# Kernel tuning notes

Hardware: AMD Instinct MI355X
Metric: run time of the kernel (lower is better)

Reference implementation:

```python
import jax, jax.numpy as jnp
import numpy as np

L, D, H, DFF = 4, 1024, 16, 4096
DH = D // H
B, T = 2, 2048
EPS = 1e-5


def setup_inputs() -> dict:
    key = jax.random.key(0)
    ks = jax.random.split(key, 16)
    xav_a = (6.0 / (D + D)) ** 0.5      # xavier_uniform for square DxD
    xav_f1 = (6.0 / (D + DFF)) ** 0.5
    xav_f2 = (6.0 / (DFF + D)) ** 0.5
    def u(k, shape, a):
        return jax.random.uniform(k, shape, jnp.float32, -a, a)
    inp = {
        "x": jax.random.normal(ks[0], (B, T, D), jnp.float32),
        "mask": jnp.ones((B, T), jnp.int32),
        # attention projections, torch Linear layout [out, in]
        "Wq": u(ks[1], (L, D, D), xav_a), "bq": jnp.zeros((L, D), jnp.float32),
        "Wk": u(ks[2], (L, D, D), xav_a), "bk": jnp.zeros((L, D), jnp.float32),
        "Wv": u(ks[3], (L, D, D), xav_a), "bv": jnp.zeros((L, D), jnp.float32),
        "Wo": u(ks[4], (L, D, D), xav_a), "bo": jnp.zeros((L, D), jnp.float32),
        # FFN
        "fc1_w": u(ks[5], (L, DFF, D), xav_f1), "fc1_b": jnp.zeros((L, DFF), jnp.float32),
        "fc2_w": u(ks[6], (L, D, DFF), xav_f2), "fc2_b": jnp.zeros((L, D), jnp.float32),
        # LayerNorms
        "ln1_g": jnp.ones((L, D), jnp.float32), "ln1_b": jnp.zeros((L, D), jnp.float32),
        "ln2_g": jnp.ones((L, D), jnp.float32), "ln2_b": jnp.zeros((L, D), jnp.float32),
        "lnf_g": jnp.ones((D,), jnp.float32), "lnf_b": jnp.zeros((D,), jnp.float32),
    }
    return inp


def _layernorm(x, g, b):
    mu = jnp.mean(x, axis=-1, keepdims=True)
    var = jnp.mean(jnp.square(x - mu), axis=-1, keepdims=True)
    return (x - mu) * jax.lax.rsqrt(var + EPS) * g + b


def _encoder_forward(x, mask, Wq, bq, Wk, bk, Wv, bv, Wo, bo,
                     fc1_w, fc1_b, fc2_w, fc2_b,
                     ln1_g, ln1_b, ln2_g, ln2_b, lnf_g, lnf_b):
    keep = mask.astype(bool)[:, None, None, :]  # [B,1,1,Tk]
    scale = 1.0 / (DH ** 0.5)
    for l in range(L):
        # --- multi-head self-attention ---
        q = (jnp.einsum('btd,ed->bte', x, Wq[l]) + bq[l]).reshape(B, T, H, DH).transpose(0, 2, 1, 3)
        k = (jnp.einsum('btd,ed->bte', x, Wk[l]) + bk[l]).reshape(B, T, H, DH).transpose(0, 2, 1, 3)
        v = (jnp.einsum('btd,ed->bte', x, Wv[l]) + bv[l]).reshape(B, T, H, DH).transpose(0, 2, 1, 3)
        logits = jnp.einsum('bhqd,bhkd->bhqk', q, k) * scale
        logits = jnp.where(keep, logits, -jnp.inf)
        attn = jax.nn.softmax(logits, axis=-1)
        ctx = jnp.einsum('bhqk,bhkd->bhqd', attn, v).transpose(0, 2, 1, 3).reshape(B, T, D)
        attn_out = jnp.einsum('btd,ed->bte', ctx, Wo[l]) + bo[l]
        x = _layernorm(x + attn_out, ln1_g[l], ln1_b[l])
        # --- feed-forward (exact GELU, like torch nn.GELU default) ---
        h = jax.nn.gelu(jnp.einsum('btd,fd->btf', x, fc1_w[l]) + fc1_b[l], approximate=False)
        ff_out = jnp.einsum('btf,df->btd', h, fc2_w[l]) + fc2_b[l]
        x = _layernorm(x + ff_out, ln2_g[l], ln2_b[l])
    return _layernorm(x, lnf_g, lnf_b)


def reference(x, mask, Wq, bq, Wk, bk, Wv, bv, Wo, bo,
              fc1_w, fc1_b, fc2_w, fc2_b,
              ln1_g, ln1_b, ln2_g, ln2_b, lnf_g, lnf_b):
    return _encoder_forward(x, mask, Wq, bq, Wk, bk, Wv, bv, Wo, bo,
                            fc1_w, fc1_b, fc2_w, fc2_b,
                            ln1_g, ln1_b, ln2_g, ln2_b, lnf_g, lnf_b)
```

## Files before the change

kernel.cpp:

```cpp
#include <hip/hip_runtime.h>
#include <hip/hip_bf16.h>
#include <cstdint>

#define BB 2
#define TT 2048
#define DD 1024
#define HH 16
#define DHH 64
#define DFF 4096
#define LL 4
#define MM (BB*TT)
#define NT (TT/64)

typedef __attribute__((ext_vector_type(8))) short short8v;
typedef __attribute__((ext_vector_type(4))) short short4v;
typedef __attribute__((ext_vector_type(4))) float floatx4;

typedef __attribute__((address_space(3))) void lds_void;
typedef const __attribute__((address_space(1))) void glb_void;

__device__ __forceinline__ void gload_lds16(const void* g, void* l) {
  __builtin_amdgcn_global_load_lds((glb_void*)g, (lds_void*)l, 16, 0, 0);
}

__device__ __forceinline__ float bf2f(short s) {
  union { unsigned u; float f; } v; v.u = ((unsigned)(unsigned short)s) << 16; return v.f;
}
__device__ __forceinline__ short f2bf(float f) {
  union { float f; unsigned u; } v; v.f = f;
  unsigned r = (v.u + 0x7fffu + ((v.u >> 16) & 1u)) >> 16;
  return (short)r;
}
__device__ __forceinline__ unsigned pack2bf(float a, float b) {
  __hip_bfloat162 h = __float22bfloat162_rn(make_float2(a, b));
  return *reinterpret_cast<unsigned*>(&h);
}
__device__ __forceinline__ float fexp2(float x) {
  float r; asm("v_exp_f32 %0, %1" : "=v"(r) : "v"(x)); return r;
}
__device__ __forceinline__ float max3f(float a, float b, float c) {
  float r; asm("v_max3_f32 %0, %1, %2, %3" : "=v"(r) : "v"(a), "v"(b), "v"(c)); return r;
}
__device__ __forceinline__ float gelu_fast(float x) {
  const float u = x * x;
  const float w = fmaf(u, -0.10294537f, -2.302203f);
  const float t = fexp2(w * x);
  return x * __builtin_amdgcn_rcpf(1.f + t);
}

#define SCL2 0.18033688011112042f
__device__ __forceinline__ short8v scale8(short8v v) {
  short8v r;
#pragma unroll
  for (int i = 0; i < 8; ++i) r[i] = f2bf(bf2f(v[i]) * SCL2);
  return r;
}

#define SEG (DD*DD)
#define WTOT (4*SEG + 2*DFF*DD)
__global__ __launch_bounds__(256) void cast_layer(
    const float* __restrict__ wq, const float* __restrict__ wk,
    const float* __restrict__ wv, const float* __restrict__ wo,
    const float* __restrict__ f1, const float* __restrict__ f2,
    short* __restrict__ dst)
{
  const int i = (blockIdx.x * 256 + threadIdx.x) * 4;
  const float* src; int off;
  if      (i <     SEG) { src = wq; off = i; }
  else if (i < 2 * SEG) { src = wk; off = i - SEG; }
  else if (i < 3 * SEG) { src = wv; off = i - 2 * SEG; }
  else if (i < 4 * SEG) { src = wo; off = i - 3 * SEG; }
  else if (i < 4 * SEG + DFF * DD) { src = f1; off = i - 4 * SEG; }
  else { src = f2; off = i - 4 * SEG - DFF * DD; }
  const float4 v = *(const float4*)(src + off);
  short4v o; o[0] = f2bf(v.x); o[1] = f2bf(v.y); o[2] = f2bf(v.z); o[3] = f2bf(v.w);
  *(short4v*)(dst + i) = o;
}

template<int GELU, int QKV>
__global__ __launch_bounds__(512, 2) void gemm256(
    const short* __restrict__ A, const short* __restrict__ W,
    const float* __restrict__ b0, const float* __restrict__ b1,
    const float* __restrict__ b2, short* __restrict__ C,
    int M, int N, int K)
{
  __shared__ __align__(16) short lds[65536];
  const int t = threadIdx.x;
  const int lane = t & 63, wave = t >> 6;
  const int wm = wave >> 2, wn = wave & 3;
  const int l15 = lane & 15, lg = lane >> 4;

  const int nwg = gridDim.x * gridDim.y;
  const int bid0 = blockIdx.y * gridDim.x + blockIdx.x;
  const int q8 = nwg >> 3;
  const int lid = (bid0 & 7) * q8 + (bid0 >> 3);
  const int bx = lid % gridDim.x, by = lid / gridDim.x;

  const size_t abase = (size_t)by * 256 * K;
  const size_t wbase = (size_t)bx * 256 * K;

  floatx4 acc[8][4];
  floatx4 zero = {0.f, 0.f, 0.f, 0.f};
#pragma unroll
  for (int m = 0; m < 8; ++m)
#pragma unroll
    for (int n = 0; n < 4; ++n) acc[m][n] = zero;

#define STG_A(sl_, h_, u_) do {                                                \
    _Pragma("unroll")                                                          \
    for (int j_ = 0; j_ < 2; ++j_) {                                           \
      const int c_ = j_ * 512 + t, r_ = c_ >> 3;                               \
      const int kc_ = (c_ & 7) ^ (r_ & 7);                                     \
      gload_lds16(A + abase + (size_t)((h_) * 128 + r_) * K + (u_) * 64 + kc_ * 8, \
                  &lds[(sl_) * 16384 + (h_) * 8192 + (j_ * 512 + wave * 64) * 8]); \
    } } while (0)
#define STG_B(sl_, h_, u_) do {                                                \
    _Pragma("unroll")                                                          \
    for (int j_ = 0; j_ < 2; ++j_) {                                           \
      const int c_ = j_ * 512 + t, r_ = c_ >> 3;                               \
      const int kc_ = (c_ & 7) ^ (r_ & 7);                                     \
      gload_lds16(W + wbase + (size_t)((h_) * 128 + r_) * K + (u_) * 64 + kc_ * 8, \
                  &lds[32768 + (sl_) * 16384 + (h_) * 8192 + (j_ * 512 + wave * 64) * 8]); \
    } } while (0)

  const int NTK = K >> 6;
  STG_A(0, 0, 0); STG_A(0, 1, 0); STG_B(0, 0, 0); STG_B(0, 1, 0);

  for (int u = 0; u < NTK; ++u) {
    const int sl = u & 1, ns = sl ^ 1;
    const int aoff = sl * 16384 + wm * 8192;
    const int boff = 32768 + sl * 16384 + (wn >> 1) * 8192;
    short8v bfr[4][2];
#pragma unroll
    for (int p = 0; p < 4; ++p) {
      if (p == 0) {
        if (u + 1 < NTK) {
          STG_A(ns, 0, u + 1);
          asm volatile("s_waitcnt vmcnt(2)" ::: "memory");
        } else {
          asm volatile("s_waitcnt vmcnt(0)" ::: "memory");
        }
        __builtin_amdgcn_s_barrier();
#pragma unroll
        for (int n = 0; n < 4; ++n)
#pragma unroll
          for (int kk = 0; kk < 2; ++kk) {
            const int rl = (wn & 1) * 64 + n * 16 + l15;
            bfr[n][kk] = *(const short8v*)&lds[boff + rl * 64 + ((kk * 4 + lg) ^ (rl & 7)) * 8];
          }
      } else if (p == 1) { if (u + 1 < NTK) STG_A(ns, 1, u + 1); }
      else if (p == 2)   { if (u + 1 < NTK) STG_B(ns, 0, u + 1); }
      else               { if (u + 1 < NTK) STG_B(ns, 1, u + 1); }

      short8v af[2][2];
#pragma unroll
      for (int i = 0; i < 2; ++i)
#pragma unroll
        for (int kk = 0; kk < 2; ++kk) {
          const int rl = (2 * p + i) * 16 + l15;
          af[i][kk] = *(const short8v*)&lds[aoff + rl * 64 + ((kk * 4 + lg) ^ (rl & 7)) * 8];
        }
      asm volatile("s_waitcnt lgkmcnt(0)" ::: "memory");
      __builtin_amdgcn_s_setprio(1);
#pragma unroll
      for (int kk = 0; kk < 2; ++kk)
#pragma unroll
        for (int i = 0; i < 2; ++i)
#pragma unroll
          for (int n = 0; n < 4; ++n)
            acc[2 * p + i][n] = __builtin_amdgcn_mfma_f32_16x16x32_bf16(
                af[i][kk], bfr[n][kk], acc[2 * p + i][n], 0, 0, 0);
      __builtin_amdgcn_s_setprio(0);
      __builtin_amdgcn_s_barrier();
    }
  }
#undef STG_A
#undef STG_B

  const float* bp;
  int cbase = bx * 256 + wn * 64;
  if (QKV) {
    const int seg = cbase >> 10;
    bp = (seg == 0) ? b0 : (seg == 1 ? b1 : b2);
    cbase -= seg << 10;
  } else {
    bp = b0;
  }
  float bv[4];
#pragma unroll
  for (int n = 0; n < 4; ++n)
    bv[n] = bp[cbase + n * 16 + l15];
#pragma unroll
  for (int m = 0; m < 8; ++m)
#pragma unroll
    for (int jj = 0; jj < 4; ++jj) {
      const int row = by * 256 + wm * 128 + m * 16 + lg * 4 + jj;
      short* cp = C + (size_t)row * N + bx * 256 + wn * 64 + l15;
#pragma unroll
      for (int n = 0; n < 4; ++n) {
        float v = acc[m][n][jj] + bv[n];
        if (GELU) v = gelu_fast(v);
        cp[n * 16] = f2bf(v);
      }
    }
}

template<int GELU>
__global__ __launch_bounds__(512, 2) void gemm128(
    const short* __restrict__ A, const short* __restrict__ W,
    const float* __restrict__ bias, short* __restrict__ C,
    int M, int N, int K)
{
  __shared__ __align__(16) short lds[49152];
  const int t = threadIdx.x;
  const int lane = t & 63, wave = t >> 6;
  const int wm = wave >> 2, wn = wave & 3;
  const int l15 = lane & 15, lg = lane >> 4;

  const int nwg = gridDim.x * gridDim.y;
  const int bid0 = blockIdx.y * gridDim.x + blockIdx.x;
  const int q8 = nwg >> 3;
  const int lid = (bid0 & 7) * q8 + (bid0 >> 3);
  const int bx = lid % gridDim.x, by = lid / gridDim.x;

  const size_t abase = (size_t)by * 128 * K;
  const size_t wbase = (size_t)bx * 128 * K;

  floatx4 acc[4][2];
  floatx4 zero = {0.f, 0.f, 0.f, 0.f};
#pragma unroll
  for (int m = 0; m < 4; ++m)
#pragma unroll
    for (int n = 0; n < 2; ++n) acc[m][n] = zero;

#define STG128(sl_, u_) do {                                                   \
    _Pragma("unroll")                                                          \
    for (int j_ = 0; j_ < 2; ++j_) {                                           \
      const int c_ = j_ * 512 + t, r_ = c_ >> 3;                               \
      const int kc_ = (c_ & 7) ^ (r_ & 7);                                     \
      gload_lds16(A + abase + (size_t)r_ * K + (u_) * 64 + kc_ * 8,            \
                  &lds[(sl_) * 8192 + (j_ * 512 + wave * 64) * 8]);            \
      gload_lds16(W + wbase + (size_t)r_ * K + (u_) * 64 + kc_ * 8,            \
                  &lds[24576 + (sl_) * 8192 + (j_ * 512 + wave * 64) * 8]);    \
    } } while (0)

  const int NTK = K >> 6;
  STG128(0, 0);
  STG128(1, 1);

  for (int u = 0; u < NTK; ++u) {
    const int sl = u % 3;
    if (u + 1 < NTK) asm volatile("s_waitcnt vmcnt(4)" ::: "memory");
    else             asm volatile("s_waitcnt vmcnt(0)" ::: "memory");
    __builtin_amdgcn_s_barrier();
    if (u + 2 < NTK) STG128((u + 2) % 3, u + 2);

    short8v bfr[2][2], af[4][2];
#pragma unroll
    for (int n = 0; n < 2; ++n)
#pragma unroll
      for (int kk = 0; kk < 2; ++kk) {
        const int rl = wn * 32 + n * 16 + l15;
        bfr[n][kk] = *(const short8v*)&lds[24576 + sl * 8192 + rl * 64 + ((kk * 4 + lg) ^ (rl & 7)) * 8];
      }
#pragma unroll
    for (int m = 0; m < 4; ++m)
#pragma unroll
      for (int kk = 0; kk < 2; ++kk) {
        const int rl = wm * 32 + ((m & 1) * 16) + l15 + (m >> 1) * 64;
        af[m][kk] = *(const short8v*)&lds[sl * 8192 + rl * 64 + ((kk * 4 + lg) ^ (rl & 7)) * 8];
      }
    asm volatile("s_waitcnt lgkmcnt(0)" ::: "memory");
    __builtin_amdgcn_s_setprio(1);
#pragma unroll
    for (int kk = 0; kk < 2; ++kk)
#pragma unroll
      for (int m = 0; m < 4; ++m)
#pragma unroll
        for (int n = 0; n < 2; ++n)
          acc[m][n] = __builtin_amdgcn_mfma_f32_16x16x32_bf16(af[m][kk], bfr[n][kk], acc[m][n], 0, 0, 0);
    __builtin_amdgcn_s_setprio(0);
  }
#undef STG128

  float bv[2];
#pragma unroll
  for (int n = 0; n < 2; ++n)
    bv[n] = bias[bx * 128 + wn * 32 + n * 16 + l15];
#pragma unroll
  for (int m = 0; m < 4; ++m)
#pragma unroll
    for (int jj = 0; jj < 4; ++jj) {
      const int row = by * 128 + wm * 32 + (m & 1) * 16 + (m >> 1) * 64 + lg * 4 + jj;
      short* cp = C + (size_t)row * N + bx * 128 + wn * 32 + l15;
#pragma unroll
      for (int n = 0; n < 2; ++n) {
        float v = acc[m][n][jj] + bv[n];
        if (GELU) v = gelu_fast(v);
        cp[n * 16] = f2bf(v);
      }
    }
}

__global__ __launch_bounds__(256) void transpose_v(
    const short* __restrict__ qkv, short* __restrict__ vt)
{
  __shared__ short tile[64][65];
  const int tb = blockIdx.x, h = blockIdx.y, b = blockIdx.z;
  const int t = threadIdx.x;
  const int r = t >> 2, c4 = (t & 3) * 16;
  const short* src = qkv + ((size_t)(b * TT + tb * 64 + r)) * 3072 + 2048 + h * 64 + c4;
#pragma unroll
  for (int i = 0; i < 16; ++i) tile[r][c4 + i] = src[i];
  __syncthreads();
  short* dst = vt + ((size_t)((b * HH + h) * 64 + r)) * TT + tb * 64 + c4;
#pragma unroll
  for (int i = 0; i < 16; ++i) dst[i] = tile[c4 + i][r];
}

#define PSTR 72
__global__ __launch_bounds__(512, 4) void flash_attn(
    const short* __restrict__ qkv, const short* __restrict__ vt,
    const int* __restrict__ mask, short* __restrict__ ctx)
{
  const int t = threadIdx.x;
  const int lane = t & 63, wave = t >> 6;
  const int l15 = lane & 15, lg = lane >> 4;

  const int bid0 = blockIdx.x + gridDim.x * (blockIdx.y + gridDim.y * blockIdx.z);
  const int lid = (bid0 & 7) * 64 + (bid0 >> 3);
  const int qb = lid & 15, h = (lid >> 4) & 15, b = lid >> 8;

  __shared__ __align__(16) short Ks[2][64 * 64];
  __shared__ __align__(16) short Vs[2][64 * 64];
  __shared__ __align__(16) short p_lds[8][16 * PSTR];
  __shared__ int allv_lds;
  short* prow = p_lds[wave];

  if (t == 0) allv_lds = 1;
  __syncthreads();
  {
    const int4 mv = *(const int4*)&mask[b * TT + t * 4];
    if (!(mv.x && mv.y && mv.z && mv.w)) allv_lds = 0;
  }
  __syncthreads();
  const bool allv = (allv_lds != 0);

  const short* qp = qkv + ((size_t)(b * TT + qb * 128 + wave * 16 + l15)) * 3072 + h * 64;
  const short8v qf0 = scale8(*(const short8v*)(qp + lg * 8));
  const short8v qf1 = scale8(*(const short8v*)(qp + 32 + lg * 8));

  const short* kbase = qkv + (size_t)b * TT * 3072 + 1024 + h * 64;
  const short* vtb   = vt + ((size_t)(b * HH + h)) * 64 * TT;

  const int srow = lane >> 3;
  const int scol = (lane & 7) ^ (srow & 7);

  float m_run = -3e30f, l_run = 0.f;
  floatx4 zero = {0.f, 0.f, 0.f, 0.f};
  floatx4 o[4];
#pragma unroll
  for (int n = 0; n < 4; ++n) o[n] = zero;

#define STAGE_KV(bufi, kb_) do {                                             \
    const int r_ = wave * 8 + srow;                                          \
    gload_lds16(kbase + (size_t)((kb_) * 64 + r_) * 3072 + scol * 8,         \
                &Ks[bufi][wave * 512]);                                      \
    gload_lds16(vtb + (size_t)r_ * TT + (kb_) * 64 + scol * 8,               \
                &Vs[bufi][wave * 512]);                                      \
  } while (0)

#define FLASH_LOOP(MASKED)                                                        \
  {                                                                               \
    STAGE_KV(0, 0);                                                               \
    int buf = 0;                                                                  \
    for (int kb = 0; kb < NT; ++kb) {                                             \
      if (kb + 1 < NT) {                                                          \
        STAGE_KV(buf ^ 1, kb + 1);                                                \
        asm volatile("s_waitcnt vmcnt(2)" ::: "memory");                          \
      } else {                                                                    \
        asm volatile("s_waitcnt vmcnt(0)" ::: "memory");                          \
      }                                                                           \
      __builtin_amdgcn_s_barrier();                                               \
                                                                                  \
      float cm[4][4];                                                             \
      if (MASKED) {                                                               \
        _Pragma("unroll")                                                         \
        for (int n = 0; n < 4; ++n) {                                             \
          const int4 mv = *(const int4*)&mask[b * TT + kb * 64 + n * 16 + lg * 4];\
          cm[n][0] = mv.x ? 0.f : -1.5e30f; cm[n][1] = mv.y ? 0.f : -1.5e30f;     \
          cm[n][2] = mv.z ? 0.f : -1.5e30f; cm[n][3] = mv.w ? 0.f : -1.5e30f;     \
        }                                                                         \
      }                                                                           \
                                                                                  \
      floatx4 s[4];                                                               \
      _Pragma("unroll")                                                           \
      for (int n = 0; n < 4; ++n) {                                               \
        const int row = n * 16 + l15;                                             \
        const int ch0 = lg ^ (row & 7);                                           \
        const int ch1 = (lg + 4) ^ (row & 7);                                     \
        const short8v kf0 = *(const short8v*)&Ks[buf][row * 64 + ch0 * 8];        \
        const short8v kf1 = *(const short8v*)&Ks[buf][row * 64 + ch1 * 8];        \
        floatx4 a = zero;                                                         \
        a = __builtin_amdgcn_mfma_f32_16x16x32_bf16(kf0, qf0, a, 0, 0, 0);        \
        a = __builtin_amdgcn_mfma_f32_16x16x32_bf16(kf1, qf1, a, 0, 0, 0);        \
        s[n] = a;                                                                 \
      }                                                                           \
      if (MASKED) {                                                               \
        _Pragma("unroll")                                                         \
        for (int n = 0; n < 4; ++n)                                               \
          _Pragma("unroll")                                                       \
          for (int jj = 0; jj < 4; ++jj) s[n][jj] += cm[n][jj];                   \
      }                                                                           \
                                                                                  \
      const float t0 = max3f(s[0][0], s[0][1], s[0][2]);                          \
      const float t1 = max3f(s[0][3], s[1][0], s[1][1]);                          \
      const float t2 = max3f(s[1][2], s[1][3], s[2][0]);                          \
      const float t3 = max3f(s[2][1], s[2][2], s[2][3]);                          \
      const float t4 = max3f(s[3][0], s[3][1], s[3][2]);                          \
      float mx = fmaxf(max3f(t0, t1, t2), max3f(t3, t4, s[3][3]));                \
      mx = fmaxf(mx, __shfl_xor(mx, 16, 64));                                     \
      mx = fmaxf(mx, __shfl_xor(mx, 32, 64));                                     \
                                                                                  \
      const bool defer = __all(mx - m_run <= 11.5f);                              \
      const float mnew = defer ? m_run : fmaxf(m_run, mx);                        \
      float ps[4];                                                                \
      _Pragma("unroll")                                                           \
      for (int n = 0; n < 4; ++n) {                                               \
        s[n][0] = fexp2(s[n][0] - mnew);                                          \
        s[n][1] = fexp2(s[n][1] - mnew);                                          \
        s[n][2] = fexp2(s[n][2] - mnew);                                          \
        s[n][3] = fexp2(s[n][3] - mnew);                                          \
        ps[n] = (s[n][0] + s[n][1]) + (s[n][2] + s[n][3]);                        \
      }                                                                           \
      float sum = (ps[0] + ps[1]) + (ps[2] + ps[3]);                              \
      sum += __shfl_xor(sum, 16, 64);                                             \
      sum += __shfl_xor(sum, 32, 64);                                             \
      if (defer) {                                                                \
        l_run += sum;                                                             \
      } else {                                                                    \
        const float al = fexp2(m_run - mnew);                                     \
        l_run = l_run * al + sum;                                                 \
        m_run = mnew;                                                             \
        float alo[4];                                                             \
        _Pragma("unroll")                                                         \
        for (int jj = 0; jj < 4; ++jj) alo[jj] = __shfl(al, lg * 4 + jj, 16);     \
        _Pragma("unroll")                                                         \
        for (int n = 0; n < 4; ++n)                                               \
          _Pragma("unroll")                                                       \
          for (int jj = 0; jj < 4; ++jj) o[n][jj] *= alo[jj];                     \
      }                                                                           \
                                                                                  \
      _Pragma("unroll")                                                           \
      for (int n = 0; n < 4; ++n) {                                               \
        const unsigned u0 = pack2bf(s[n][0], s[n][1]);                            \
        const unsigned u1 = pack2bf(s[n][2], s[n][3]);                            \
        *(uint2*)&prow[l15 * PSTR + n * 16 + lg * 4] = make_uint2(u0, u1);        \
      }                                                                           \
      const short8v pf0 = *(const short8v*)&prow[l15 * PSTR + lg * 8];            \
      const short8v pf1 = *(const short8v*)&prow[l15 * PSTR + 32 + lg * 8];       \
                                                                                  \
      _Pragma("unroll")                                                           \
      for (int n = 0; n < 4; ++n) {                                               \
        const int row = n * 16 + l15;                                             \
        const int ch0 = lg ^ (row & 7);                                           \
        const int ch1 = (lg + 4) ^ (row & 7);                                     \
        const short8v vf0 = *(const short8v*)&Vs[buf][row * 64 + ch0 * 8];        \
        const short8v vf1 = *(const short8v*)&Vs[buf][row * 64 + ch1 * 8];        \
        o[n] = __builtin_amdgcn_mfma_f32_16x16x32_bf16(pf0, vf0, o[n], 0, 0, 0);  \
        o[n] = __builtin_amdgcn_mfma_f32_16x16x32_bf16(pf1, vf1, o[n], 0, 0, 0);  \
      }                                                                           \
      asm volatile("" ::: "memory");                                              \
      __builtin_amdgcn_s_barrier();                                               \
      buf ^= 1;                                                                   \
    }                                                                             \
  }

  if (allv) FLASH_LOOP(0)
  else      FLASH_LOOP(1)
#undef FLASH_LOOP
#undef STAGE_KV

#pragma unroll
  for (int jj = 0; jj < 4; ++jj) {
    const float inv = 1.f / __shfl(l_run, lg * 4 + jj, 16);
    const int row = qb * 128 + wave * 16 + lg * 4 + jj;
#pragma unroll
    for (int n = 0; n < 4; ++n)
      ctx[((size_t)(b * TT + row)) * DD + h * 64 + n * 16 + l15] = f2bf(o[n][jj] * inv);
  }
}

__global__ __launch_bounds__(256) void add_ln(
    const float* __restrict__ xres, const short* __restrict__ add,
    const float* __restrict__ g, const float* __restrict__ bb,
    float* __restrict__ outf, short* __restrict__ outb)
{
  const int row = blockIdx.x, t = threadIdx.x;
  const int lane = t & 63, wave = t >> 6;
  const float4 xv = *(const float4*)(xres + (size_t)row * DD + t * 4);
  float y[4] = { xv.x, xv.y, xv.z, xv.w };
  if (add) {
    const short4v av = *(const short4v*)(add + (size_t)row * DD + t * 4);
#pragma unroll
    for (int i = 0; i < 4; ++i) y[i] += bf2f(av[i]);
  }
  float s = y[0] + y[1] + y[2] + y[3];
  float ss = y[0]*y[0] + y[1]*y[1] + y[2]*y[2] + y[3]*y[3];
#pragma unroll
  for (int off = 32; off >= 1; off >>= 1) {
    s  += __shfl_xor(s, off, 64);
    ss += __shfl_xor(ss, off, 64);
  }
  __shared__ float red[2][4];
  if (lane == 0) { red[0][wave] = s; red[1][wave] = ss; }
  __syncthreads();
  s  = red[0][0] + red[0][1] + red[0][2] + red[0][3];
  ss = red[1][0] + red[1][1] + red[1][2] + red[1][3];
  const float mu = s * (1.f / DD);
  const float var = ss * (1.f / DD) - mu * mu;
  const float rs = rsqrtf(var + 1e-5f);
  const float4 gv = *(const float4*)(g + t * 4);
  const float4 bv = *(const float4*)(bb + t * 4);
  float o[4];
  o[0] = (y[0] - mu) * rs * gv.x + bv.x;
  o[1] = (y[1] - mu) * rs * gv.y + bv.y;
  o[2] = (y[2] - mu) * rs * gv.z + bv.z;
  o[3] = (y[3] - mu) * rs * gv.w + bv.w;
  if (outf) *(float4*)(outf + (size_t)row * DD + t * 4) = make_float4(o[0], o[1], o[2], o[3]);
  if (outb) {
    short4v ov;
#pragma unroll
    for (int i = 0; i < 4; ++i) ov[i] = f2bf(o[i]);
    *(short4v*)(outb + (size_t)row * DD + t * 4) = ov;
  }
}

__global__ __launch_bounds__(256) void cast_in(
    const float* __restrict__ x, short* __restrict__ xb)
{
  const int i = (blockIdx.x * 256 + threadIdx.x) * 4;
  const float4 v = *(const float4*)(x + i);
  short4v o; o[0] = f2bf(v.x); o[1] = f2bf(v.y); o[2] = f2bf(v.z); o[3] = f2bf(v.w);
  *(short4v*)(xb + i) = o;
}

extern "C" void kernel_launch(void* const* d_in, const int* in_sizes, int n_in,
                              void* d_out, int out_size, void* d_ws, size_t ws_size,
                              hipStream_t stream) {
  const float* x   = (const float*)d_in[0];
  const int* mask  = (const int*)d_in[1];
  const float* Wq  = (const float*)d_in[2];
  const float* bq  = (const float*)d_in[3];
  const float* Wk  = (const float*)d_in[4];
  const float* bk  = (const float*)d_in[5];
  const float* Wv  = (const float*)d_in[6];
  const float* bv  = (const float*)d_in[7];
  const float* Wo  = (const float*)d_in[8];
  const float* bo  = (const float*)d_in[9];
  const float* f1w = (const float*)d_in[10];
  const float* f1b = (const float*)d_in[11];
  const float* f2w = (const float*)d_in[12];
  const float* f2b = (const float*)d_in[13];
  const float* l1g = (const float*)d_in[14];
  const float* l1b = (const float*)d_in[15];
  const float* l2g = (const float*)d_in[16];
  const float* l2b = (const float*)d_in[17];
  const float* lfg = (const float*)d_in[18];
  const float* lfb = (const float*)d_in[19];
  float* out = (float*)d_out;

  char* ws = (char*)d_ws;
  const size_t MB = 1u << 20;
  float* xf   = (float*)(ws);
  short* xb   = (short*)(ws + 16 * MB);
  short* qkv  = (short*)(ws + 24 * MB);
  short* vt_  = (short*)(ws + 48 * MB);
  short* ctx  = (short*)(ws + 56 * MB);
  short* tmp  = (short*)(ws + 64 * MB);
  short* wbuf = (short*)(ws + 72 * MB);
  short* hb   = qkv;

  cast_in<<<(MM * DD) / (256 * 4), 256, 0, stream>>>(x, xb);

  for (int l = 0; l < LL; ++l) {
    cast_layer<<<WTOT / (256 * 4), 256, 0, stream>>>(
        Wq + (size_t)l * SEG, Wk + (size_t)l * SEG, Wv + (size_t)l * SEG, Wo + (size_t)l * SEG,
        f1w + (size_t)l * DFF * DD, f2w + (size_t)l * DD * DFF, wbuf);
    const short* wqkv_b = wbuf;
    const short* wo_b   = wbuf + 3 * SEG;
    const short* f1_b   = wbuf + 4 * SEG;
    const short* f2_b   = wbuf + 4 * SEG + DFF * DD;

    gemm256<0,1><<<dim3(3072 / 256, MM / 256), 512, 0, stream>>>(
        xb, wqkv_b, bq + l * DD, bk + l * DD, bv + l * DD, qkv, MM, 3072, DD);
    transpose_v<<<dim3(TT / 64, HH, BB), 256, 0, stream>>>(qkv, vt_);
    flash_attn<<<dim3(TT / 128, HH, BB), 512, 0, stream>>>(qkv, vt_, mask, ctx);
    gemm128<0><<<dim3(DD / 128, MM / 128), 512, 0, stream>>>(ctx, wo_b, bo + l * DD, tmp, MM, DD, DD);
    add_ln<<<MM, 256, 0, stream>>>(l == 0 ? x : xf, tmp, l1g + l * DD, l1b + l * DD, xf, xb);
    gemm256<1,0><<<dim3(DFF / 256, MM / 256), 512, 0, stream>>>(
        xb, f1_b, f1b + l * DFF, nullptr, nullptr, hb, MM, DFF, DD);
    gemm128<0><<<dim3(DD / 128, MM / 128), 512, 0, stream>>>(hb, f2_b, f2b + l * DD, tmp, MM, DD, DFF);
    add_ln<<<MM, 256, 0, stream>>>(xf, tmp, l2g + l * DD, l2b + l * DD, xf, xb);
  }
  add_ln<<<MM, 256, 0, stream>>>(xf, nullptr, lfg, lfb, out, nullptr);
}
```

Before: 907.0 us.

## Fuse V transpose into QKV GEMM epilogue and keep residual stream in bf16

The QKV GEMM epilogue now writes the V columns directly in transposed [b,h,dh,t] layout, so the separate transpose_v kernel and its extra read/write pass go away. The fp32 residual buffer is also dropped: add_ln reads and writes the residual only in bf16, which cuts memory traffic per LayerNorm. In exchange, the QKV GEMM does extra scattered 8-byte stores for V tiles, and keeping the residual in bf16 lowers accuracy across layers.

```diff
diff --git a/kernel.cpp b/kernel.cpp
--- a/kernel.cpp
+++ b/kernel.cpp
@@ -82,6 +82,7 @@
     const short* __restrict__ A, const short* __restrict__ W,
     const float* __restrict__ b0, const float* __restrict__ b1,
     const float* __restrict__ b2, short* __restrict__ C,
+    short* __restrict__ VT,
     int M, int N, int K)
 {
   __shared__ __align__(16) short lds[65536];
@@ -203,6 +204,22 @@
         cp[n * 16] = f2bf(v);
       }
     }
+
+  if (QKV && bx >= 8) {
+#pragma unroll
+    for (int m = 0; m < 8; ++m) {
+      const int row0 = by * 256 + wm * 128 + m * 16 + lg * 4;
+      const int b_ = row0 >> 11, t_ = row0 & (TT - 1);
+#pragma unroll
+      for (int n = 0; n < 4; ++n) {
+        const int hdh = bx * 256 + wn * 64 + n * 16 + l15 - 2048;
+        short4v ov;
+#pragma unroll
+        for (int jj = 0; jj < 4; ++jj) ov[jj] = f2bf(acc[m][n][jj] + bv[n]);
+        *(short4v*)(VT + ((size_t)(b_ * 1024 + hdh)) * TT + t_) = ov;
+      }
+    }
+  }
 }
 
 template<int GELU>
@@ -300,22 +317,6 @@
         cp[n * 16] = f2bf(v);
       }
     }
-}
-
-__global__ __launch_bounds__(256) void transpose_v(
-    const short* __restrict__ qkv, short* __restrict__ vt)
-{
-  __shared__ short tile[64][65];
-  const int tb = blockIdx.x, h = blockIdx.y, b = blockIdx.z;
-  const int t = threadIdx.x;
-  const int r = t >> 2, c4 = (t & 3) * 16;
-  const short* src = qkv + ((size_t)(b * TT + tb * 64 + r)) * 3072 + 2048 + h * 64 + c4;
-#pragma unroll
-  for (int i = 0; i < 16; ++i) tile[r][c4 + i] = src[i];
-  __syncthreads();
-  short* dst = vt + ((size_t)((b * HH + h) * 64 + r)) * TT + tb * 64 + c4;
-#pragma unroll
-  for (int i = 0; i < 16; ++i) dst[i] = tile[c4 + i][r];
 }
 
 #define PSTR 72
@@ -491,15 +492,24 @@
   }
 }
 
+template<int XF32, int OUTF>
 __global__ __launch_bounds__(256) void add_ln(
-    const float* __restrict__ xres, const short* __restrict__ add,
+    const float* __restrict__ xrf, const short* __restrict__ xrb,
+    const short* __restrict__ add,
     const float* __restrict__ g, const float* __restrict__ bb,
     float* __restrict__ outf, short* __restrict__ outb)
 {
   const int row = blockIdx.x, t = threadIdx.x;
   const int lane = t & 63, wave = t >> 6;
-  const float4 xv = *(const float4*)(xres + (size_t)row * DD + t * 4);
-  float y[4] = { xv.x, xv.y, xv.z, xv.w };
+  float y[4];
+  if (XF32) {
+    const float4 xv = *(const float4*)(xrf + (size_t)row * DD + t * 4);
+    y[0] = xv.x; y[1] = xv.y; y[2] = xv.z; y[3] = xv.w;
+  } else {
+    const short4v xv = *(const short4v*)(xrb + (size_t)row * DD + t * 4);
+#pragma unroll
+    for (int i = 0; i < 4; ++i) y[i] = bf2f(xv[i]);
+  }
   if (add) {
     const short4v av = *(const short4v*)(add + (size_t)row * DD + t * 4);
 #pragma unroll
@@ -527,8 +537,9 @@
   o[1] = (y[1] - mu) * rs * gv.y + bv.y;
   o[2] = (y[2] - mu) * rs * gv.z + bv.z;
   o[3] = (y[3] - mu) * rs * gv.w + bv.w;
-  if (outf) *(float4*)(outf + (size_t)row * DD + t * 4) = make_float4(o[0], o[1], o[2], o[3]);
-  if (outb) {
+  if (OUTF) {
+    *(float4*)(outf + (size_t)row * DD + t * 4) = make_float4(o[0], o[1], o[2], o[3]);
+  } else {
     short4v ov;
 #pragma unroll
     for (int i = 0; i < 4; ++i) ov[i] = f2bf(o[i]);
@@ -537,12 +548,12 @@
 }
 
 __global__ __launch_bounds__(256) void cast_in(
-    const float* __restrict__ x, short* __restrict__ xb)
+    const float* __restrict__ x, short* __restrict__ xr)
 {
   const int i = (blockIdx.x * 256 + threadIdx.x) * 4;
   const float4 v = *(const float4*)(x + i);
   short4v o; o[0] = f2bf(v.x); o[1] = f2bf(v.y); o[2] = f2bf(v.z); o[3] = f2bf(v.w);
-  *(short4v*)(xb + i) = o;
+  *(short4v*)(xr + i) = o;
 }
 
 extern "C" void kernel_launch(void* const* d_in, const int* in_sizes, int n_in,
@@ -572,16 +583,15 @@
 
   char* ws = (char*)d_ws;
   const size_t MB = 1u << 20;
-  float* xf   = (float*)(ws);
-  short* xb   = (short*)(ws + 16 * MB);
-  short* qkv  = (short*)(ws + 24 * MB);
-  short* vt_  = (short*)(ws + 48 * MB);
-  short* ctx  = (short*)(ws + 56 * MB);
-  short* tmp  = (short*)(ws + 64 * MB);
-  short* wbuf = (short*)(ws + 72 * MB);
+  short* xr   = (short*)(ws);
+  short* qkv  = (short*)(ws + 8 * MB);
+  short* vt_  = (short*)(ws + 32 * MB);
+  short* ctx  = (short*)(ws + 40 * MB);
+  short* tmp  = (short*)(ws + 48 * MB);
+  short* wbuf = (short*)(ws + 56 * MB);
   short* hb   = qkv;
 
-  cast_in<<<(MM * DD) / (256 * 4), 256, 0, stream>>>(x, xb);
+  cast_in<<<(MM * DD) / (256 * 4), 256, 0, stream>>>(x, xr);
 
   for (int l = 0; l < LL; ++l) {
     cast_layer<<<WTOT / (256 * 4), 256, 0, stream>>>(
@@ -593,15 +603,17 @@
     const short* f2_b   = wbuf + 4 * SEG + DFF * DD;
 
     gemm256<0,1><<<dim3(3072 / 256, MM / 256), 512, 0, stream>>>(
-        xb, wqkv_b, bq + l * DD, bk + l * DD, bv + l * DD, qkv, MM, 3072, DD);
-    transpose_v<<<dim3(TT / 64, HH, BB), 256, 0, stream>>>(qkv, vt_);
+        xr, wqkv_b, bq + l * DD, bk + l * DD, bv + l * DD, qkv, vt_, MM, 3072, DD);
     flash_attn<<<dim3(TT / 128, HH, BB), 512, 0, stream>>>(qkv, vt_, mask, ctx);
     gemm128<0><<<dim3(DD / 128, MM / 128), 512, 0, stream>>>(ctx, wo_b, bo + l * DD, tmp, MM, DD, DD);
-    add_ln<<<MM, 256, 0, stream>>>(l == 0 ? x : xf, tmp, l1g + l * DD, l1b + l * DD, xf, xb);
+    if (l == 0)
+      add_ln<1,0><<<MM, 256, 0, stream>>>(x, nullptr, tmp, l1g, l1b, nullptr, xr);
+    else
+      add_ln<0,0><<<MM, 256, 0, stream>>>(nullptr, xr, tmp, l1g + l * DD, l1b + l * DD, nullptr, xr);
     gemm256<1,0><<<dim3(DFF / 256, MM / 256), 512, 0, stream>>>(
-        xb, f1_b, f1b + l * DFF, nullptr, nullptr, hb, MM, DFF, DD);
+        xr, f1_b, f1b + l * DFF, nullptr, nullptr, hb, nullptr, MM, DFF, DD);
     gemm128<0><<<dim3(DD / 128, MM / 128), 512, 0, stream>>>(hb, f2_b, f2b + l * DD, tmp, MM, DD, DFF);
-    add_ln<<<MM, 256, 0, stream>>>(xf, tmp, l2g + l * DD, l2b + l * DD, xf, xb);
-  }
-  add_ln<<<MM, 256, 0, stream>>>(xf, nullptr, lfg, lfb, out, nullptr);
-}
+    add_ln<0,0><<<MM, 256, 0, stream>>>(nullptr, xr, tmp, l2g + l * DD, l2b + l * DD, nullptr, xr);
+  }
+  add_ln<0,1><<<MM, 256, 0, stream>>>(nullptr, xr, nullptr, lfg, lfb, out, nullptr);
+}
```

New measurement: 880.3 us. 1.03x faster.
